# Optimization experiments

Measured on AMD Instinct MI355X. Metric: run time of the kernel, lower is better.

Reference implementation:

```python
import jax, jax.numpy as jnp
import numpy as np

EPS = 1e-10
WS = 5  # window_size
PAD = WS // 2


def _conv(x, k, pad_h, pad_w):
    # x: [N,1,H,W], k: [1,1,kh,kw], 'same'-style explicit padding
    return jax.lax.conv_general_dilated(
        x, k, window_strides=(1, 1),
        padding=[(pad_h, pad_h), (pad_w, pad_w)],
        dimension_numbers=("NCHW", "OIHW", "NCHW"))


def setup_inputs() -> dict:
    key = jax.random.key(0)
    B, C, Fr, T = 8, 2, 256, 2048
    spectrogram = jax.random.normal(key, (B, C, Fr, T), dtype=jnp.float32)
    # Gaussian kernel (window_size=5, sigma=1.0)
    c = WS // 2
    coords = jnp.arange(WS, dtype=jnp.float32) - c
    yy, xx = jnp.meshgrid(coords, coords, indexing="ij")
    g = jnp.exp(-(xx ** 2 + yy ** 2) / 2.0)
    gaussian_kernel = (g / g.sum()).reshape(1, 1, WS, WS)
    # Sobel kernels / 8
    sobel_x = (jnp.array([[-1, 0, 1], [-2, 0, 2], [-1, 0, 1]], jnp.float32) / 8.0).reshape(1, 1, 3, 3)
    sobel_y = (jnp.array([[-1, -2, -1], [0, 0, 0], [1, 2, 1]], jnp.float32) / 8.0).reshape(1, 1, 3, 3)
    # Harmonic kernel: 7x1 [-1,0,0,2,0,0,-1]
    hk = jnp.zeros(7, jnp.float32).at[0].set(-1.0).at[3].set(2.0).at[6].set(-1.0)
    harmonic_kernel = hk.reshape(1, 1, 7, 1)
    return {"spectrogram": spectrogram, "gaussian_kernel": gaussian_kernel,
            "sobel_x": sobel_x, "sobel_y": sobel_y, "harmonic_kernel": harmonic_kernel}


def _forward(spectrogram, gaussian_kernel, sobel_x, sobel_y, harmonic_kernel):
    B, C, Fr, T = spectrogram.shape
    # Per-channel 1-in/1-out convs == fold channels into batch.
    x = spectrogram.reshape(B * C, 1, Fr, T)

    grad_freq = _conv(x, sobel_y, 1, 1)
    grad_time = _conv(x, sobel_x, 1, 1)
    magnitude = jnp.sqrt(grad_freq ** 2 + grad_time ** 2 + EPS)
    angle = jnp.arctan2(grad_freq, grad_time + EPS)

    # ---- entropy (structure-tensor eigenvalue entropy) ----
    vx = magnitude * jnp.cos(angle)
    vy = magnitude * jnp.sin(angle)
    vxx = _conv(vx * vx, gaussian_kernel, PAD, PAD)
    vyy = _conv(vy * vy, gaussian_kernel, PAD, PAD)
    vxy = _conv(vx * vy, gaussian_kernel, PAD, PAD)
    trace = vxx + vyy
    det = vxx * vyy - vxy * vxy
    disc = jnp.sqrt(jnp.maximum(trace * trace - 4.0 * det, 0.0) + EPS)
    l1 = jnp.maximum((trace + disc) / 2.0, EPS)
    l2 = jnp.maximum((trace - disc) / 2.0, EPS)
    s = l1 + l2 + EPS
    p1, p2 = l1 / s, l2 / s
    entropy = -(p1 * jnp.log(p1 + EPS) + p2 * jnp.log(p2 + EPS)) / np.log(2.0)
    entropy = jnp.clip(entropy, 0.0, 1.0)

    # ---- alignment ----
    ux = jnp.cos(angle)
    uy = jnp.sin(angle)
    ux_avg = _conv(ux, gaussian_kernel, PAD, PAD)
    uy_avg = _conv(uy, gaussian_kernel, PAD, PAD)
    alignment = jnp.clip(jnp.sqrt(ux_avg ** 2 + uy_avg ** 2 + EPS), 0.0, 1.0)

    # ---- curvature ----
    dudx = _conv(ux, sobel_x, 1, 1)
    dudy = _conv(ux, sobel_y, 1, 1)
    dvdx = _conv(uy, sobel_x, 1, 1)
    dvdy = _conv(uy, sobel_y, 1, 1)
    curv = jnp.sqrt(dudx ** 2 + dudy ** 2 + dvdx ** 2 + dvdy ** 2 + EPS)
    curvature = _conv(curv, gaussian_kernel, PAD, PAD)

    # ---- harmonic coherence ----
    harm = jnp.abs(_conv(x, harmonic_kernel, 3, 0))
    local_energy = _conv(x ** 2, gaussian_kernel, PAD, PAD)
    harmonic = jnp.clip(harm / (local_energy + EPS), 0.0, 1.0)

    # ---- temporal stability: inverse temporal gradient magnitude, smoothed ----
    temporal = _conv(1.0 / (1.0 + jnp.abs(grad_time)), gaussian_kernel, PAD, PAD)
    temporal = jnp.clip(temporal, 0.0, 1.0)

    # ---- spectral flow: smoothed frequency-gradient magnitude ----
    spectral = jnp.clip(_conv(jnp.abs(grad_freq), gaussian_kernel, PAD, PAD), 0.0, 1.0)

    def chan_mean(f):  # [B*C,1,F,T] -> [B,1,F,T]
        return f.reshape(B, C, Fr, T).mean(axis=1, keepdims=True)

    return (chan_mean(entropy), chan_mean(alignment), chan_mean(curvature),
            chan_mean(harmonic), chan_mean(temporal), chan_mean(spectral))


def reference(spectrogram, gaussian_kernel, sobel_x, sobel_y, harmonic_kernel):
    return _forward(spectrogram, gaussian_kernel, sobel_x, sobel_y, harmonic_kernel)
```

## Files before the change

kernel.cpp:

```cpp
#include <hip/hip_runtime.h>
#include <hip/hip_fp16.h>


#define F_DIM 256
#define T_DIM 2048
#define B_DIM 8
#define C_DIM 2
#define TILE  32
#define NTHR  512

#define XROWS 40
#define XS    40
#define UROWS 38
#define US    40
#define FROWS 36
#define FS    36
#define FH2   18
#define EPSF  1e-10f

template<bool V> struct BoolC { static constexpr bool value = V; };

static __device__ __forceinline__ __half2 pack_h2(float a, float b) {
    auto v = __builtin_amdgcn_cvt_pkrtz(a, b);
    return *(__half2*)&v;
}
static __device__ __forceinline__ float clamp01(float x) {
    return fminf(fmaxf(x, 0.f), 1.f);
}

__global__ __launch_bounds__(512, 4)
void audio_struct_fused(const float* __restrict__ x_in,
                        const float* __restrict__ gk_in,
                        float* __restrict__ out)
{
    __shared__ __align__(16) float   s_x [XROWS*XS];
    __shared__ __align__(16) __half2 s_u [UROWS*US];
    __shared__ __align__(16) __half2 s_P0[FROWS*FS];
    __shared__ __align__(16) __half2 s_P1[FROWS*FS];
    __shared__ __align__(16) __half2 s_P2[FROWS*FS];
    __shared__ __align__(16) __half2 s_P3[FROWS*FS];
    __shared__ __align__(16) float   s_tmp[TILE*FS];

    const int tx  = threadIdx.x;
    const int ty  = threadIdx.y;
    const int tid = ty * 32 + tx;
    const int t0  = blockIdx.x * TILE;
    const int f0  = blockIdx.y * TILE;
    const int b   = blockIdx.z;

    float r0 = gk_in[10], r1 = gk_in[11], r2 = gk_in[12], r3 = gk_in[13], r4 = gk_in[14];
    float winv = __builtin_amdgcn_rcpf(r0 + r1 + r2 + r3 + r4);
    const float w[5] = {r0*winv, r1*winv, r2*winv, r3*winv, r4*winv};
    const __half2 wh2[5] = {pack_h2(w[0],w[0]), pack_h2(w[1],w[1]), pack_h2(w[2],w[2]),
                            pack_h2(w[3],w[3]), pack_h2(w[4],w[4])};
    const __half2 h2z    = pack_h2(0.f, 0.f);
    const __half2 two    = pack_h2(2.f, 2.f);
    const __half2 eighth = pack_h2(0.125f, 0.125f);

    auto vpass_pair = [&](const __half2* src, __half2* dst) {
        const uint2* s = (const uint2*)src;
        uint2* d = (uint2*)dst;
        for (int idx = tid; idx < TILE * FH2; idx += NTHR) {
            __half2 a0 = h2z, a1 = h2z;
            #pragma unroll
            for (int i = 0; i < 5; ++i) {
                uint2 v = s[idx + i * FH2];
                a0 = __hfma2(wh2[i], *(const __half2*)&v.x, a0);
                a1 = __hfma2(wh2[i], *(const __half2*)&v.y, a1);
            }
            uint2 o; o.x = *(const unsigned*)&a0; o.y = *(const unsigned*)&a1;
            d[idx] = o;
        }
    };

    float acc[6][2];
    #pragma unroll
    for (int k = 0; k < 6; ++k)
        #pragma unroll
        for (int s = 0; s < 2; ++s) acc[k][s] = 0.0f;

    const bool interior = (f0 >= 4) && (f0 + TILE + 4 <= F_DIM) &&
                          (t0 >= 4) && (t0 + TILE + 4 <= T_DIM);

    auto phaseABC = [&](const float* xp, auto FASTC) {
        constexpr bool FAST = decltype(FASTC)::value;

        for (int idx = tid; idx < XROWS * 20; idx += NTHR) {
            int r  = idx / 20, c2 = idx - r * 20;
            float2 v;
            if (FAST) {
                v = *(const float2*)(xp + (size_t)(f0 + r - 4) * T_DIM + (t0 + c2 * 2 - 4));
            } else {
                int gf = f0 + r - 4;
                int gt = t0 + c2 * 2 - 4;
                v = make_float2(0.f, 0.f);
                if ((unsigned)gf < (unsigned)F_DIM && (unsigned)gt < (unsigned)T_DIM)
                    v = *(const float2*)(xp + (size_t)gf * T_DIM + gt);
            }
            *(float2*)&s_x[r * XS + c2 * 2] = v;
        }
        __syncthreads();

        for (int q = tid; q < UROWS * 19; q += NTHR) {
            int r = q / 19, m = q - r * 19;
            const float2* x2p = (const float2*)s_x;
            int base = r * (XS/2) + m;
            float2 a0 = x2p[base],            b0 = x2p[base + 1];
            float2 a1 = x2p[base + (XS/2)],   b1 = x2p[base + (XS/2) + 1];
            float2 a2 = x2p[base + XS],       b2 = x2p[base + XS + 1];
            float c0 = a2.x - a0.x, c1 = a2.y - a0.y;
            float c2c = b2.x - b0.x, c3 = b2.y - b0.y;
            float s0 = fmaf(2.f, a1.x, a0.x + a2.x);
            float s1 = fmaf(2.f, a1.y, a0.y + a2.y);
            float s2 = fmaf(2.f, b1.x, b0.x + b2.x);
            float s3 = fmaf(2.f, b1.y, b0.y + b2.y);
            float gfvA = (fmaf(2.f, c1, c0) + c2c) * 0.125f;
            float gtvA = (s2 - s0) * 0.125f;
            float gfvB = (fmaf(2.f, c2c, c1) + c3) * 0.125f;
            float gtvB = (s3 - s1) * 0.125f;

            bool rin = (r >= 1) && (r < UROWS - 1);
            int  fiA = (r - 1) * FS + 2 * m - 1;
            int  gfr = f0 + r - 3;
            bool frOK = FAST || ((unsigned)gfr < (unsigned)F_DIM);

            #pragma unroll
            for (int jj = 0; jj < 2; ++jj) {
                float gfv = jj ? gfvB : gfvA;
                float gtv = jj ? gtvB : gtvA;
                int   ccI = 2 * m + jj;
                bool  okI = true;
                if (!FAST) {
                    int gtc = t0 + ccI - 3;
                    okI = frOK & ((unsigned)gtc < (unsigned)T_DIM);
                }
                float ux = 0.f, uy = 0.f, trp = 0.f, dfp = 0.f, sxy = 0.f,
                      tin = 0.f, sf = 0.f;
                if (okI) {
                    float gte = gtv + EPSF;
                    float g2f = gfv * gfv;
                    float d2  = fmaf(gte, gte, g2f);
                    float rh  = __builtin_amdgcn_rsqf(d2);
                    ux = gte * rh;
                    uy = gfv * rh;
                    float m2 = fmaf(gtv, gtv, g2f) + EPSF;
                    trp = m2;
                    dfp = m2 * (ux - uy) * (ux + uy);
                    sxy = m2 * ux * uy;
                    tin = __builtin_amdgcn_rcpf(1.0f + fabsf(gtv));
                    sf  = fabsf(gfv);
                }
                s_u[r * US + ccI + 1] = pack_h2(ux, uy);
                bool pv = rin && (jj ? (m <= 17) : (m >= 1));
                if (pv) {
                    int fi = fiA + jj;
                    s_P0[fi] = pack_h2(trp, dfp);
                    s_P1[fi] = pack_h2(sxy, tin);
                    s_P2[fi] = pack_h2(sf, 0.f);
                }
            }
        }
        __syncthreads();

        for (int q = tid; q < FROWS * 18; q += NTHR) {
            int r = q / 18, m = q - r * 18;
            const uint2* su2 = (const uint2*)s_u;
            int base = r * (US/2) + m;
            uint2 q00 = su2[base],              q01 = su2[base + 1],              q02 = su2[base + 2];
            uint2 q10 = su2[base + (US/2)],     q11 = su2[base + (US/2) + 1],     q12 = su2[base + (US/2) + 2];
            uint2 q20 = su2[base + US],         q21 = su2[base + US + 1],         q22 = su2[base + US + 2];
            #define H2(v) (*(const __half2*)&(v))
            __half2 l1 = __hadd2(H2(q00.y), H2(q20.y)); l1 = __hfma2(two, H2(q10.y), l1);
            __half2 l2 = __hadd2(H2(q01.x), H2(q21.x)); l2 = __hfma2(two, H2(q11.x), l2);
            __half2 l3 = __hadd2(H2(q01.y), H2(q21.y)); l3 = __hfma2(two, H2(q11.y), l3);
            __half2 l4 = __hadd2(H2(q02.x), H2(q22.x)); l4 = __hfma2(two, H2(q12.x), l4);
            __half2 tA = __hadd2(H2(q00.y), H2(q01.y)); tA = __hfma2(two, H2(q01.x), tA);
            __half2 bA = __hadd2(H2(q20.y), H2(q21.y)); bA = __hfma2(two, H2(q21.x), bA);
            __half2 tB = __hadd2(H2(q01.x), H2(q02.x)); tB = __hfma2(two, H2(q01.y), tB);
            __half2 bB = __hadd2(H2(q21.x), H2(q22.x)); bB = __hfma2(two, H2(q21.y), bB);
            #undef H2
            __half2 dxA = __hmul2(__hsub2(l3, l1), eighth);
            __half2 dyA = __hmul2(__hsub2(bA, tA), eighth);
            __half2 dxB = __hmul2(__hsub2(l4, l2), eighth);
            __half2 dyB = __hmul2(__hsub2(bB, tB), eighth);

            int gfr = f0 + r - 2;
            bool frOK = FAST || ((unsigned)gfr < (unsigned)F_DIM);
            #pragma unroll
            for (int jj = 0; jj < 2; ++jj) {
                float2 fx = __half22float2(jj ? dxB : dxA);
                float2 fy = __half22float2(jj ? dyB : dyA);
                float cv = __builtin_amdgcn_sqrtf(
                    fmaf(fx.x, fx.x, fmaf(fx.y, fx.y,
                    fmaf(fy.x, fy.x, fy.y * fy.y))) + EPSF);
                int ccI = 2 * m + jj;
                if (!FAST) {
                    int gtc = t0 + ccI - 2;
                    if (!(frOK & ((unsigned)gtc < (unsigned)T_DIM))) cv = 0.f;
                }
                ((__half*)s_P2)[2 * (r * FS + ccI) + 1] = __float2half_rn(cv);
            }
        }
        vpass_pair(s_P0, (__half2*)s_tmp);
        vpass_pair(s_P1, s_P3);
        __syncthreads();
    };

    for (int c = 0; c < C_DIM; ++c) {
        if (c) __syncthreads();

        const float* xp = x_in + (size_t)(b * C_DIM + c) * F_DIM * T_DIM;
        if (interior) phaseABC(xp, BoolC<true>{});
        else          phaseABC(xp, BoolC<false>{});

        __half2* tmp_h2 = (__half2*)s_tmp;

        {
            float trace_s[2], diff_s[2];
            #pragma unroll
            for (int s = 0; s < 2; ++s) {
                int ry = ty + 16 * s;
                float a = 0.f, bv = 0.f;
                #pragma unroll
                for (int j = 0; j < 5; ++j) {
                    float2 v = __half22float2(tmp_h2[ry * FS + tx + j]);
                    a += w[j] * v.x; bv += w[j] * v.y;
                }
                trace_s[s] = a; diff_s[s] = bv;
            }
            #pragma unroll
            for (int s = 0; s < 2; ++s) {
                int ry = ty + 16 * s;
                __half2 a = h2z;
                #pragma unroll
                for (int j = 0; j < 5; ++j)
                    a = __hfma2(wh2[j], s_P3[ry * FS + tx + j], a);
                float2 v = __half22float2(a);
                float trace = trace_s[s], diff = diff_s[s];
                float disc  = __builtin_amdgcn_sqrtf(
                                  fmaxf(diff * diff + 4.f * v.x * v.x, 0.f) + EPSF);
                float l1 = fmaxf(0.5f * (trace + disc), EPSF);
                float l2 = fmaxf(0.5f * (trace - disc), EPSF);
                float inv = __builtin_amdgcn_rcpf(l1 + l2 + EPSF);
                float p1 = l1 * inv, p2 = l2 * inv;
                float ent = -(p1 * __builtin_amdgcn_logf(p1 + EPSF)
                            + p2 * __builtin_amdgcn_logf(p2 + EPSF));
                acc[0][s] += 0.5f * clamp01(ent);
                acc[4][s] += 0.5f * clamp01(v.y);
            }
            vpass_pair(s_P2, s_P0);
            {
                const uint2* su2 = (const uint2*)s_u;
                uint2* dP1 = (uint2*)s_P1;
                for (int idx = tid; idx < TILE * FH2; idx += NTHR) {
                    int r = idx / FH2, p = idx - r * FH2;
                    const uint2* sp = su2 + (r + 1) * (US/2) + 1 + p;
                    __half2 a0 = h2z, a1 = h2z;
                    #pragma unroll
                    for (int i = 0; i < 5; ++i) {
                        uint2 v = sp[i * (US/2)];
                        a0 = __hfma2(wh2[i], *(const __half2*)&v.x, a0);
                        a1 = __hfma2(wh2[i], *(const __half2*)&v.y, a1);
                    }
                    uint2 o; o.x = *(const unsigned*)&a0; o.y = *(const unsigned*)&a1;
                    dP1[idx] = o;
                }
            }
        }
        __syncthreads();

        #pragma unroll
        for (int s = 0; s < 2; ++s) {
            int ry = ty + 16 * s;
            __half2 a = h2z;
            #pragma unroll
            for (int j = 0; j < 5; ++j)
                a = __hfma2(wh2[j], s_P0[ry * FS + tx + j], a);
            float2 v = __half22float2(a);
            acc[5][s] += 0.5f * clamp01(v.x);
            acc[2][s] += 0.5f * v.y;
        }
        #pragma unroll
        for (int s = 0; s < 2; ++s) {
            int ry = ty + 16 * s;
            __half2 a = h2z;
            #pragma unroll
            for (int j = 0; j < 5; ++j)
                a = __hfma2(wh2[j], s_P1[ry * FS + tx + j], a);
            float2 v = __half22float2(a);
            acc[1][s] += 0.5f * clamp01(
                __builtin_amdgcn_sqrtf(v.x * v.x + v.y * v.y + EPSF));
        }
        {
            const float2* sx2 = (const float2*)s_x;
            float2* dt2 = (float2*)s_tmp;
            for (int idx = tid; idx < TILE * FH2; idx += NTHR) {
                int r = idx / FH2, p = idx - r * FH2;
                const float2* sp = sx2 + (r + 2) * (XS/2) + 1 + p;
                float a = 0.f, bv = 0.f;
                #pragma unroll
                for (int i = 0; i < 5; ++i) {
                    float2 v = sp[i * (XS/2)];
                    a  = fmaf(w[i], v.x * v.x, a);
                    bv = fmaf(w[i], v.y * v.y, bv);
                }
                dt2[idx] = make_float2(a, bv);
            }
        }
        __syncthreads();

        #pragma unroll
        for (int s = 0; s < 2; ++s) {
            int ry = ty + 16 * s;
            float le = 0.f;
            #pragma unroll
            for (int j = 0; j < 5; ++j)
                le += w[j] * s_tmp[ry * FS + tx + j];
            float xm  = s_x[(ry + 1) * XS + tx + 4];
            float x0v = s_x[(ry + 4) * XS + tx + 4];
            float xpv = s_x[(ry + 7) * XS + tx + 4];
            float harm = fabsf(2.f * x0v - xm - xpv);
            acc[3][s] += 0.5f * clamp01(harm * __builtin_amdgcn_rcpf(le + EPSF));
        }
    }

    const size_t plane = (size_t)B_DIM * F_DIM * T_DIM;
    const size_t base  = (size_t)b * F_DIM * T_DIM + (size_t)f0 * T_DIM + t0 + tx;
    #pragma unroll
    for (int k = 0; k < 6; ++k)
        #pragma unroll
        for (int s = 0; s < 2; ++s)
            out[k * plane + base + (size_t)(ty + 16 * s) * T_DIM] = acc[k][s];
}

extern "C" void kernel_launch(void* const* d_in, const int* in_sizes, int n_in,
                              void* d_out, int out_size, void* d_ws, size_t ws_size,
                              hipStream_t stream) {
    const float* x  = (const float*)d_in[0];
    const float* gk = (const float*)d_in[1];
    float* out = (float*)d_out;
    dim3 grid(T_DIM / TILE, F_DIM / TILE, B_DIM);
    dim3 block(32, 16);
    audio_struct_fused<<<grid, block, 0, stream>>>(x, gk, out);
}
```

Measured before the change: 206.3 us.

## Give each thread two adjacent columns and two rows for register reuse

Changes thread-to-output mapping so each thread computes two horizontally adjacent outputs (one row, two columns) in the horizontal passes, reusing loaded shared-memory values across both outputs via wide uint2/float2 loads. The vertical passes now produce two output rows per thread from six loaded rows instead of five per row. Final stores become float2 writes. Intent is to cut LDS load count and instruction overhead; it raises register pressure under a 512x4 launch bound.

Measured after the change: 202.0 us. 2.1% less time.

```diff
diff --git a/kernel.cpp b/kernel.cpp
--- a/kernel.cpp
+++ b/kernel.cpp
@@ -26,6 +26,9 @@
 }
 static __device__ __forceinline__ float clamp01(float x) {
     return fminf(fmaxf(x, 0.f), 1.f);
+}
+static __device__ __forceinline__ __half2 u2h(unsigned v) {
+    return *(const __half2*)&v;
 }
 
 __global__ __launch_bounds__(512, 4)
@@ -44,6 +47,8 @@
     const int tx  = threadIdx.x;
     const int ty  = threadIdx.y;
     const int tid = ty * 32 + tx;
+    const int ryh = tid >> 4;
+    const int mch = tid & 15;
     const int t0  = blockIdx.x * TILE;
     const int f0  = blockIdx.y * TILE;
     const int b   = blockIdx.z;
@@ -57,19 +62,27 @@
     const __half2 two    = pack_h2(2.f, 2.f);
     const __half2 eighth = pack_h2(0.125f, 0.125f);
 
-    auto vpass_pair = [&](const __half2* src, __half2* dst) {
+    auto vpass2 = [&](const __half2* src, __half2* dst) {
         const uint2* s = (const uint2*)src;
         uint2* d = (uint2*)dst;
-        for (int idx = tid; idx < TILE * FH2; idx += NTHR) {
-            __half2 a0 = h2z, a1 = h2z;
+        for (int idx = tid; idx < 16 * FH2; idx += NTHR) {
+            int rg = idx / FH2, p = idx - rg * FH2;
+            int base = 2 * rg * FH2 + p;
+            uint2 vv[6];
+            #pragma unroll
+            for (int i = 0; i < 6; ++i) vv[i] = s[base + i * FH2];
+            __half2 a0 = h2z, a1 = h2z, b0 = h2z, b1 = h2z;
             #pragma unroll
             for (int i = 0; i < 5; ++i) {
-                uint2 v = s[idx + i * FH2];
-                a0 = __hfma2(wh2[i], *(const __half2*)&v.x, a0);
-                a1 = __hfma2(wh2[i], *(const __half2*)&v.y, a1);
-            }
-            uint2 o; o.x = *(const unsigned*)&a0; o.y = *(const unsigned*)&a1;
-            d[idx] = o;
+                a0 = __hfma2(wh2[i], u2h(vv[i].x),     a0);
+                a1 = __hfma2(wh2[i], u2h(vv[i].y),     a1);
+                b0 = __hfma2(wh2[i], u2h(vv[i + 1].x), b0);
+                b1 = __hfma2(wh2[i], u2h(vv[i + 1].y), b1);
+            }
+            uint2 oa; oa.x = *(const unsigned*)&a0; oa.y = *(const unsigned*)&a1;
+            uint2 ob; ob.x = *(const unsigned*)&b0; ob.y = *(const unsigned*)&b1;
+            d[base] = oa;
+            d[base + FH2] = ob;
         }
     };
 
@@ -169,16 +182,14 @@
             uint2 q00 = su2[base],              q01 = su2[base + 1],              q02 = su2[base + 2];
             uint2 q10 = su2[base + (US/2)],     q11 = su2[base + (US/2) + 1],     q12 = su2[base + (US/2) + 2];
             uint2 q20 = su2[base + US],         q21 = su2[base + US + 1],         q22 = su2[base + US + 2];
-            #define H2(v) (*(const __half2*)&(v))
-            __half2 l1 = __hadd2(H2(q00.y), H2(q20.y)); l1 = __hfma2(two, H2(q10.y), l1);
-            __half2 l2 = __hadd2(H2(q01.x), H2(q21.x)); l2 = __hfma2(two, H2(q11.x), l2);
-            __half2 l3 = __hadd2(H2(q01.y), H2(q21.y)); l3 = __hfma2(two, H2(q11.y), l3);
-            __half2 l4 = __hadd2(H2(q02.x), H2(q22.x)); l4 = __hfma2(two, H2(q12.x), l4);
-            __half2 tA = __hadd2(H2(q00.y), H2(q01.y)); tA = __hfma2(two, H2(q01.x), tA);
-            __half2 bA = __hadd2(H2(q20.y), H2(q21.y)); bA = __hfma2(two, H2(q21.x), bA);
-            __half2 tB = __hadd2(H2(q01.x), H2(q02.x)); tB = __hfma2(two, H2(q01.y), tB);
-            __half2 bB = __hadd2(H2(q21.x), H2(q22.x)); bB = __hfma2(two, H2(q21.y), bB);
-            #undef H2
+            __half2 l1 = __hadd2(u2h(q00.y), u2h(q20.y)); l1 = __hfma2(two, u2h(q10.y), l1);
+            __half2 l2 = __hadd2(u2h(q01.x), u2h(q21.x)); l2 = __hfma2(two, u2h(q11.x), l2);
+            __half2 l3 = __hadd2(u2h(q01.y), u2h(q21.y)); l3 = __hfma2(two, u2h(q11.y), l3);
+            __half2 l4 = __hadd2(u2h(q02.x), u2h(q22.x)); l4 = __hfma2(two, u2h(q12.x), l4);
+            __half2 tA = __hadd2(u2h(q00.y), u2h(q01.y)); tA = __hfma2(two, u2h(q01.x), tA);
+            __half2 bA = __hadd2(u2h(q20.y), u2h(q21.y)); bA = __hfma2(two, u2h(q21.x), bA);
+            __half2 tB = __hadd2(u2h(q01.x), u2h(q02.x)); tB = __hfma2(two, u2h(q01.y), tB);
+            __half2 bB = __hadd2(u2h(q21.x), u2h(q22.x)); bB = __hfma2(two, u2h(q21.y), bB);
             __half2 dxA = __hmul2(__hsub2(l3, l1), eighth);
             __half2 dyA = __hmul2(__hsub2(bA, tA), eighth);
             __half2 dxB = __hmul2(__hsub2(l4, l2), eighth);
@@ -201,8 +212,8 @@
                 ((__half*)s_P2)[2 * (r * FS + ccI) + 1] = __float2half_rn(cv);
             }
         }
-        vpass_pair(s_P0, (__half2*)s_tmp);
-        vpass_pair(s_P1, s_P3);
+        vpass2(s_P0, (__half2*)s_tmp);
+        vpass2(s_P1, s_P3);
         __syncthreads();
     };
 
@@ -216,27 +227,37 @@
         __half2* tmp_h2 = (__half2*)s_tmp;
 
         {
-            float trace_s[2], diff_s[2];
-            #pragma unroll
-            for (int s = 0; s < 2; ++s) {
-                int ry = ty + 16 * s;
-                float a = 0.f, bv = 0.f;
-                #pragma unroll
-                for (int j = 0; j < 5; ++j) {
-                    float2 v = __half22float2(tmp_h2[ry * FS + tx + j]);
-                    a += w[j] * v.x; bv += w[j] * v.y;
-                }
-                trace_s[s] = a; diff_s[s] = bv;
-            }
-            #pragma unroll
-            for (int s = 0; s < 2; ++s) {
-                int ry = ty + 16 * s;
-                __half2 a = h2z;
-                #pragma unroll
-                for (int j = 0; j < 5; ++j)
-                    a = __hfma2(wh2[j], s_P3[ry * FS + tx + j], a);
-                float2 v = __half22float2(a);
-                float trace = trace_s[s], diff = diff_s[s];
+            const uint2* t2 = (const uint2*)tmp_h2;
+            uint2 ta = t2[ryh * FH2 + mch], tb = t2[ryh * FH2 + mch + 1],
+                  tc = t2[ryh * FH2 + mch + 2];
+            float2 e0 = __half22float2(u2h(ta.x)), e1 = __half22float2(u2h(ta.y));
+            float2 e2 = __half22float2(u2h(tb.x)), e3 = __half22float2(u2h(tb.y));
+            float2 e4 = __half22float2(u2h(tc.x)), e5 = __half22float2(u2h(tc.y));
+            float trc[2], dfc[2];
+            trc[0] = w[0]*e0.x + w[1]*e1.x + w[2]*e2.x + w[3]*e3.x + w[4]*e4.x;
+            dfc[0] = w[0]*e0.y + w[1]*e1.y + w[2]*e2.y + w[3]*e3.y + w[4]*e4.y;
+            trc[1] = w[0]*e1.x + w[1]*e2.x + w[2]*e3.x + w[3]*e4.x + w[4]*e5.x;
+            dfc[1] = w[0]*e1.y + w[1]*e2.y + w[2]*e3.y + w[3]*e4.y + w[4]*e5.y;
+
+            const uint2* p3q = (const uint2*)s_P3;
+            uint2 pa = p3q[ryh * FH2 + mch], pb = p3q[ryh * FH2 + mch + 1],
+                  pc = p3q[ryh * FH2 + mch + 2];
+            __half2 aA = h2z, aB = h2z;
+            aA = __hfma2(wh2[0], u2h(pa.x), aA);
+            aA = __hfma2(wh2[1], u2h(pa.y), aA);
+            aA = __hfma2(wh2[2], u2h(pb.x), aA);
+            aA = __hfma2(wh2[3], u2h(pb.y), aA);
+            aA = __hfma2(wh2[4], u2h(pc.x), aA);
+            aB = __hfma2(wh2[0], u2h(pa.y), aB);
+            aB = __hfma2(wh2[1], u2h(pb.x), aB);
+            aB = __hfma2(wh2[2], u2h(pb.y), aB);
+            aB = __hfma2(wh2[3], u2h(pc.x), aB);
+            aB = __hfma2(wh2[4], u2h(pc.y), aB);
+            float2 vc[2] = {__half22float2(aA), __half22float2(aB)};
+            #pragma unroll
+            for (int col = 0; col < 2; ++col) {
+                float trace = trc[col], diff = dfc[col];
+                float2 v = vc[col];
                 float disc  = __builtin_amdgcn_sqrtf(
                                   fmaxf(diff * diff + 4.f * v.x * v.x, 0.f) + EPSF);
                 float l1 = fmaxf(0.5f * (trace + disc), EPSF);
@@ -245,92 +266,124 @@
                 float p1 = l1 * inv, p2 = l2 * inv;
                 float ent = -(p1 * __builtin_amdgcn_logf(p1 + EPSF)
                             + p2 * __builtin_amdgcn_logf(p2 + EPSF));
-                acc[0][s] += 0.5f * clamp01(ent);
-                acc[4][s] += 0.5f * clamp01(v.y);
-            }
-            vpass_pair(s_P2, s_P0);
+                acc[0][col] += 0.5f * clamp01(ent);
+                acc[4][col] += 0.5f * clamp01(v.y);
+            }
+
+            vpass2(s_P2, s_P0);
             {
                 const uint2* su2 = (const uint2*)s_u;
                 uint2* dP1 = (uint2*)s_P1;
-                for (int idx = tid; idx < TILE * FH2; idx += NTHR) {
-                    int r = idx / FH2, p = idx - r * FH2;
-                    const uint2* sp = su2 + (r + 1) * (US/2) + 1 + p;
-                    __half2 a0 = h2z, a1 = h2z;
+                for (int idx = tid; idx < 16 * FH2; idx += NTHR) {
+                    int rg = idx / FH2, p = idx - rg * FH2;
+                    const uint2* sp = su2 + (2 * rg + 1) * (US/2) + 1 + p;
+                    uint2 vv[6];
+                    #pragma unroll
+                    for (int i = 0; i < 6; ++i) vv[i] = sp[i * (US/2)];
+                    __half2 a0 = h2z, a1 = h2z, b0 = h2z, b1 = h2z;
                     #pragma unroll
                     for (int i = 0; i < 5; ++i) {
-                        uint2 v = sp[i * (US/2)];
-                        a0 = __hfma2(wh2[i], *(const __half2*)&v.x, a0);
-                        a1 = __hfma2(wh2[i], *(const __half2*)&v.y, a1);
+                        a0 = __hfma2(wh2[i], u2h(vv[i].x),     a0);
+                        a1 = __hfma2(wh2[i], u2h(vv[i].y),     a1);
+                        b0 = __hfma2(wh2[i], u2h(vv[i + 1].x), b0);
+                        b1 = __hfma2(wh2[i], u2h(vv[i + 1].y), b1);
                     }
-                    uint2 o; o.x = *(const unsigned*)&a0; o.y = *(const unsigned*)&a1;
-                    dP1[idx] = o;
-                }
-            }
-        }
-        __syncthreads();
-
-        #pragma unroll
-        for (int s = 0; s < 2; ++s) {
-            int ry = ty + 16 * s;
-            __half2 a = h2z;
-            #pragma unroll
-            for (int j = 0; j < 5; ++j)
-                a = __hfma2(wh2[j], s_P0[ry * FS + tx + j], a);
-            float2 v = __half22float2(a);
-            acc[5][s] += 0.5f * clamp01(v.x);
-            acc[2][s] += 0.5f * v.y;
-        }
-        #pragma unroll
-        for (int s = 0; s < 2; ++s) {
-            int ry = ty + 16 * s;
-            __half2 a = h2z;
-            #pragma unroll
-            for (int j = 0; j < 5; ++j)
-                a = __hfma2(wh2[j], s_P1[ry * FS + tx + j], a);
-            float2 v = __half22float2(a);
-            acc[1][s] += 0.5f * clamp01(
-                __builtin_amdgcn_sqrtf(v.x * v.x + v.y * v.y + EPSF));
-        }
+                    uint2 oa; oa.x = *(const unsigned*)&a0; oa.y = *(const unsigned*)&a1;
+                    uint2 ob; ob.x = *(const unsigned*)&b0; ob.y = *(const unsigned*)&b1;
+                    dP1[2 * rg * FH2 + p] = oa;
+                    dP1[(2 * rg + 1) * FH2 + p] = ob;
+                }
+            }
+        }
+        __syncthreads();
+
         {
+            const uint2* p0q = (const uint2*)s_P0;
+            uint2 qa = p0q[ryh * FH2 + mch], qb = p0q[ryh * FH2 + mch + 1],
+                  qc = p0q[ryh * FH2 + mch + 2];
+            __half2 sA = h2z, sB = h2z;
+            sA = __hfma2(wh2[0], u2h(qa.x), sA);
+            sA = __hfma2(wh2[1], u2h(qa.y), sA);
+            sA = __hfma2(wh2[2], u2h(qb.x), sA);
+            sA = __hfma2(wh2[3], u2h(qb.y), sA);
+            sA = __hfma2(wh2[4], u2h(qc.x), sA);
+            sB = __hfma2(wh2[0], u2h(qa.y), sB);
+            sB = __hfma2(wh2[1], u2h(qb.x), sB);
+            sB = __hfma2(wh2[2], u2h(qb.y), sB);
+            sB = __hfma2(wh2[3], u2h(qc.x), sB);
+            sB = __hfma2(wh2[4], u2h(qc.y), sB);
+            float2 s0 = __half22float2(sA), s1 = __half22float2(sB);
+            acc[5][0] += 0.5f * clamp01(s0.x);  acc[2][0] += 0.5f * s0.y;
+            acc[5][1] += 0.5f * clamp01(s1.x);  acc[2][1] += 0.5f * s1.y;
+
+            const uint2* p1q = (const uint2*)s_P1;
+            uint2 ra = p1q[ryh * FH2 + mch], rb = p1q[ryh * FH2 + mch + 1],
+                  rc = p1q[ryh * FH2 + mch + 2];
+            __half2 uA = h2z, uB = h2z;
+            uA = __hfma2(wh2[0], u2h(ra.x), uA);
+            uA = __hfma2(wh2[1], u2h(ra.y), uA);
+            uA = __hfma2(wh2[2], u2h(rb.x), uA);
+            uA = __hfma2(wh2[3], u2h(rb.y), uA);
+            uA = __hfma2(wh2[4], u2h(rc.x), uA);
+            uB = __hfma2(wh2[0], u2h(ra.y), uB);
+            uB = __hfma2(wh2[1], u2h(rb.x), uB);
+            uB = __hfma2(wh2[2], u2h(rb.y), uB);
+            uB = __hfma2(wh2[3], u2h(rc.x), uB);
+            uB = __hfma2(wh2[4], u2h(rc.y), uB);
+            float2 u0 = __half22float2(uA), u1 = __half22float2(uB);
+            acc[1][0] += 0.5f * clamp01(
+                __builtin_amdgcn_sqrtf(u0.x * u0.x + u0.y * u0.y + EPSF));
+            acc[1][1] += 0.5f * clamp01(
+                __builtin_amdgcn_sqrtf(u1.x * u1.x + u1.y * u1.y + EPSF));
+
             const float2* sx2 = (const float2*)s_x;
             float2* dt2 = (float2*)s_tmp;
-            for (int idx = tid; idx < TILE * FH2; idx += NTHR) {
-                int r = idx / FH2, p = idx - r * FH2;
-                const float2* sp = sx2 + (r + 2) * (XS/2) + 1 + p;
-                float a = 0.f, bv = 0.f;
+            for (int idx = tid; idx < 16 * FH2; idx += NTHR) {
+                int rg = idx / FH2, p = idx - rg * FH2;
+                const float2* sp = sx2 + (2 * rg + 2) * (XS/2) + 1 + p;
+                float2 sq[6];
+                #pragma unroll
+                for (int i = 0; i < 6; ++i) {
+                    float2 v = sp[i * (XS/2)];
+                    sq[i] = make_float2(v.x * v.x, v.y * v.y);
+                }
+                float aA = 0.f, bA = 0.f, aB = 0.f, bB = 0.f;
                 #pragma unroll
                 for (int i = 0; i < 5; ++i) {
-                    float2 v = sp[i * (XS/2)];
-                    a  = fmaf(w[i], v.x * v.x, a);
-                    bv = fmaf(w[i], v.y * v.y, bv);
-                }
-                dt2[idx] = make_float2(a, bv);
-            }
-        }
-        __syncthreads();
-
-        #pragma unroll
-        for (int s = 0; s < 2; ++s) {
-            int ry = ty + 16 * s;
-            float le = 0.f;
-            #pragma unroll
-            for (int j = 0; j < 5; ++j)
-                le += w[j] * s_tmp[ry * FS + tx + j];
-            float xm  = s_x[(ry + 1) * XS + tx + 4];
-            float x0v = s_x[(ry + 4) * XS + tx + 4];
-            float xpv = s_x[(ry + 7) * XS + tx + 4];
-            float harm = fabsf(2.f * x0v - xm - xpv);
-            acc[3][s] += 0.5f * clamp01(harm * __builtin_amdgcn_rcpf(le + EPSF));
+                    aA = fmaf(w[i], sq[i].x,     aA);
+                    bA = fmaf(w[i], sq[i].y,     bA);
+                    aB = fmaf(w[i], sq[i + 1].x, aB);
+                    bB = fmaf(w[i], sq[i + 1].y, bB);
+                }
+                dt2[2 * rg * FH2 + p] = make_float2(aA, bA);
+                dt2[(2 * rg + 1) * FH2 + p] = make_float2(aB, bB);
+            }
+        }
+        __syncthreads();
+
+        {
+            const float2* tf = (const float2*)s_tmp;
+            float2 q0 = tf[ryh * FH2 + mch], q1 = tf[ryh * FH2 + mch + 1],
+                   q2 = tf[ryh * FH2 + mch + 2];
+            float le0 = w[0]*q0.x + w[1]*q0.y + w[2]*q1.x + w[3]*q1.y + w[4]*q2.x;
+            float le1 = w[0]*q0.y + w[1]*q1.x + w[2]*q1.y + w[3]*q2.x + w[4]*q2.y;
+            const float2* sxf = (const float2*)s_x;
+            float2 xm  = sxf[(ryh + 1) * (XS/2) + mch + 2];
+            float2 x0v = sxf[(ryh + 4) * (XS/2) + mch + 2];
+            float2 xpv = sxf[(ryh + 7) * (XS/2) + mch + 2];
+            float hA = fabsf(2.f * x0v.x - xm.x - xpv.x);
+            float hB = fabsf(2.f * x0v.y - xm.y - xpv.y);
+            acc[3][0] += 0.5f * clamp01(hA * __builtin_amdgcn_rcpf(le0 + EPSF));
+            acc[3][1] += 0.5f * clamp01(hB * __builtin_amdgcn_rcpf(le1 + EPSF));
         }
     }
 
     const size_t plane = (size_t)B_DIM * F_DIM * T_DIM;
-    const size_t base  = (size_t)b * F_DIM * T_DIM + (size_t)f0 * T_DIM + t0 + tx;
+    const size_t base  = (size_t)b * F_DIM * T_DIM
+                       + (size_t)(f0 + ryh) * T_DIM + t0 + 2 * mch;
     #pragma unroll
     for (int k = 0; k < 6; ++k)
-        #pragma unroll
-        for (int s = 0; s < 2; ++s)
-            out[k * plane + base + (size_t)(ty + 16 * s) * T_DIM] = acc[k][s];
+        *(float2*)(out + k * plane + base) = make_float2(acc[k][0], acc[k][1]);
 }
 
 extern "C" void kernel_launch(void* const* d_in, const int* in_sizes, int n_in,
```

## Register-block horizontal and vertical passes with 128-bit LDS accesses

Applied to the files above, without the earlier changes.

Reworks the shared-memory convolution passes so each thread computes several outputs. Vertical passes now produce two rows per thread and the Sobel pass produces four columns, using uint4/float4 LDS loads and reusing overlapping taps. Horizontal passes have only half the threads compute four adjacent outputs each, with float4 output stores. This reduces LDS load instructions and index arithmetic, at the cost of idling half the threads in the final stages and higher register pressure under the 512x4 launch bound.

Result: no change. 205.4 us (-0.5%).

```diff
diff --git a/kernel.cpp b/kernel.cpp
--- a/kernel.cpp
+++ b/kernel.cpp
@@ -16,6 +16,7 @@
 #define FROWS 36
 #define FS    36
 #define FH2   18
+#define FH4   9
 #define EPSF  1e-10f
 
 template<bool V> struct BoolC { static constexpr bool value = V; };
@@ -26,6 +27,9 @@
 }
 static __device__ __forceinline__ float clamp01(float x) {
     return fminf(fmaxf(x, 0.f), 1.f);
+}
+static __device__ __forceinline__ __half2 u2h(unsigned v) {
+    return *(const __half2*)&v;
 }
 
 __global__ __launch_bounds__(512, 4)
@@ -44,6 +48,9 @@
     const int tx  = threadIdx.x;
     const int ty  = threadIdx.y;
     const int tid = ty * 32 + tx;
+    const bool hact = (tid < 256);
+    const int ryq = tid >> 3;
+    const int mq  = tid & 7;
     const int t0  = blockIdx.x * TILE;
     const int f0  = blockIdx.y * TILE;
     const int b   = blockIdx.z;
@@ -57,27 +64,40 @@
     const __half2 two    = pack_h2(2.f, 2.f);
     const __half2 eighth = pack_h2(0.125f, 0.125f);
 
-    auto vpass_pair = [&](const __half2* src, __half2* dst) {
-        const uint2* s = (const uint2*)src;
-        uint2* d = (uint2*)dst;
-        for (int idx = tid; idx < TILE * FH2; idx += NTHR) {
-            __half2 a0 = h2z, a1 = h2z;
+    auto vpass4 = [&](const __half2* src, __half2* dst) {
+        const uint4* s = (const uint4*)src;
+        uint4* d = (uint4*)dst;
+        for (int idx = tid; idx < 16 * FH4; idx += NTHR) {
+            int rg = idx / FH4, p = idx - rg * FH4;
+            int base = 2 * rg * FH4 + p;
+            uint4 vv[6];
+            #pragma unroll
+            for (int i = 0; i < 6; ++i) vv[i] = s[base + i * FH4];
+            __half2 a0=h2z,a1=h2z,a2=h2z,a3=h2z, b0=h2z,b1=h2z,b2=h2z,b3=h2z;
             #pragma unroll
             for (int i = 0; i < 5; ++i) {
-                uint2 v = s[idx + i * FH2];
-                a0 = __hfma2(wh2[i], *(const __half2*)&v.x, a0);
-                a1 = __hfma2(wh2[i], *(const __half2*)&v.y, a1);
-            }
-            uint2 o; o.x = *(const unsigned*)&a0; o.y = *(const unsigned*)&a1;
-            d[idx] = o;
+                a0 = __hfma2(wh2[i], u2h(vv[i].x),   a0);
+                a1 = __hfma2(wh2[i], u2h(vv[i].y),   a1);
+                a2 = __hfma2(wh2[i], u2h(vv[i].z),   a2);
+                a3 = __hfma2(wh2[i], u2h(vv[i].w),   a3);
+                b0 = __hfma2(wh2[i], u2h(vv[i+1].x), b0);
+                b1 = __hfma2(wh2[i], u2h(vv[i+1].y), b1);
+                b2 = __hfma2(wh2[i], u2h(vv[i+1].z), b2);
+                b3 = __hfma2(wh2[i], u2h(vv[i+1].w), b3);
+            }
+            uint4 oa, ob;
+            oa.x=*(unsigned*)&a0; oa.y=*(unsigned*)&a1; oa.z=*(unsigned*)&a2; oa.w=*(unsigned*)&a3;
+            ob.x=*(unsigned*)&b0; ob.y=*(unsigned*)&b1; ob.z=*(unsigned*)&b2; ob.w=*(unsigned*)&b3;
+            d[base] = oa;
+            d[base + FH4] = ob;
         }
     };
 
-    float acc[6][2];
+    float acc[6][4];
     #pragma unroll
     for (int k = 0; k < 6; ++k)
         #pragma unroll
-        for (int s = 0; s < 2; ++s) acc[k][s] = 0.0f;
+        for (int s = 0; s < 4; ++s) acc[k][s] = 0.0f;
 
     const bool interior = (f0 >= 4) && (f0 + TILE + 4 <= F_DIM) &&
                           (t0 >= 4) && (t0 + TILE + 4 <= T_DIM);
@@ -162,47 +182,48 @@
         }
         __syncthreads();
 
-        for (int q = tid; q < FROWS * 18; q += NTHR) {
-            int r = q / 18, m = q - r * 18;
-            const uint2* su2 = (const uint2*)s_u;
-            int base = r * (US/2) + m;
-            uint2 q00 = su2[base],              q01 = su2[base + 1],              q02 = su2[base + 2];
-            uint2 q10 = su2[base + (US/2)],     q11 = su2[base + (US/2) + 1],     q12 = su2[base + (US/2) + 2];
-            uint2 q20 = su2[base + US],         q21 = su2[base + US + 1],         q22 = su2[base + US + 2];
-            #define H2(v) (*(const __half2*)&(v))
-            __half2 l1 = __hadd2(H2(q00.y), H2(q20.y)); l1 = __hfma2(two, H2(q10.y), l1);
-            __half2 l2 = __hadd2(H2(q01.x), H2(q21.x)); l2 = __hfma2(two, H2(q11.x), l2);
-            __half2 l3 = __hadd2(H2(q01.y), H2(q21.y)); l3 = __hfma2(two, H2(q11.y), l3);
-            __half2 l4 = __hadd2(H2(q02.x), H2(q22.x)); l4 = __hfma2(two, H2(q12.x), l4);
-            __half2 tA = __hadd2(H2(q00.y), H2(q01.y)); tA = __hfma2(two, H2(q01.x), tA);
-            __half2 bA = __hadd2(H2(q20.y), H2(q21.y)); bA = __hfma2(two, H2(q21.x), bA);
-            __half2 tB = __hadd2(H2(q01.x), H2(q02.x)); tB = __hfma2(two, H2(q01.y), tB);
-            __half2 bB = __hadd2(H2(q21.x), H2(q22.x)); bB = __hfma2(two, H2(q21.y), bB);
-            #undef H2
-            __half2 dxA = __hmul2(__hsub2(l3, l1), eighth);
-            __half2 dyA = __hmul2(__hsub2(bA, tA), eighth);
-            __half2 dxB = __hmul2(__hsub2(l4, l2), eighth);
-            __half2 dyB = __hmul2(__hsub2(bB, tB), eighth);
-
+        for (int q = tid; q < FROWS * FH4; q += NTHR) {
+            int r = q / FH4, Q = q - r * FH4;
+            const uint4* su4 = (const uint4*)s_u;
+            int base = r * 10 + Q;
+            uint4 ta4 = su4[base],      tb4 = su4[base + 1];
+            uint4 ma4 = su4[base + 10], mb4 = su4[base + 11];
+            uint4 ba4 = su4[base + 20], bb4 = su4[base + 21];
+            __half2 t_[8] = {u2h(ta4.x),u2h(ta4.y),u2h(ta4.z),u2h(ta4.w),
+                             u2h(tb4.x),u2h(tb4.y),u2h(tb4.z),u2h(tb4.w)};
+            __half2 m_[8] = {u2h(ma4.x),u2h(ma4.y),u2h(ma4.z),u2h(ma4.w),
+                             u2h(mb4.x),u2h(mb4.y),u2h(mb4.z),u2h(mb4.w)};
+            __half2 b_[8] = {u2h(ba4.x),u2h(ba4.y),u2h(ba4.z),u2h(ba4.w),
+                             u2h(bb4.x),u2h(bb4.y),u2h(bb4.z),u2h(bb4.w)};
+            __half2 l_[7];
+            #pragma unroll
+            for (int k = 1; k <= 6; ++k) {
+                __half2 s = __hadd2(t_[k], b_[k]);
+                l_[k] = __hfma2(two, m_[k], s);
+            }
             int gfr = f0 + r - 2;
             bool frOK = FAST || ((unsigned)gfr < (unsigned)F_DIM);
             #pragma unroll
-            for (int jj = 0; jj < 2; ++jj) {
-                float2 fx = __half22float2(jj ? dxB : dxA);
-                float2 fy = __half22float2(jj ? dyB : dyA);
+            for (int jj = 0; jj < 4; ++jj) {
+                __half2 tr = __hadd2(t_[jj+1], t_[jj+3]); tr = __hfma2(two, t_[jj+2], tr);
+                __half2 br = __hadd2(b_[jj+1], b_[jj+3]); br = __hfma2(two, b_[jj+2], br);
+                __half2 dx = __hmul2(__hsub2(l_[jj+3], l_[jj+1]), eighth);
+                __half2 dy = __hmul2(__hsub2(br, tr), eighth);
+                float2 fx = __half22float2(dx);
+                float2 fy = __half22float2(dy);
                 float cv = __builtin_amdgcn_sqrtf(
                     fmaf(fx.x, fx.x, fmaf(fx.y, fx.y,
                     fmaf(fy.x, fy.x, fy.y * fy.y))) + EPSF);
-                int ccI = 2 * m + jj;
+                int cc = 4 * Q + jj;
                 if (!FAST) {
-                    int gtc = t0 + ccI - 2;
+                    int gtc = t0 + cc - 2;
                     if (!(frOK & ((unsigned)gtc < (unsigned)T_DIM))) cv = 0.f;
                 }
-                ((__half*)s_P2)[2 * (r * FS + ccI) + 1] = __float2half_rn(cv);
-            }
-        }
-        vpass_pair(s_P0, (__half2*)s_tmp);
-        vpass_pair(s_P1, s_P3);
+                ((__half*)s_P2)[2 * (r * FS + cc) + 1] = __float2half_rn(cv);
+            }
+        }
+        vpass4(s_P0, (__half2*)s_tmp);
+        vpass4(s_P1, s_P3);
         __syncthreads();
     };
 
@@ -215,28 +236,30 @@
 
         __half2* tmp_h2 = (__half2*)s_tmp;
 
-        {
-            float trace_s[2], diff_s[2];
-            #pragma unroll
-            for (int s = 0; s < 2; ++s) {
-                int ry = ty + 16 * s;
-                float a = 0.f, bv = 0.f;
-                #pragma unroll
-                for (int j = 0; j < 5; ++j) {
-                    float2 v = __half22float2(tmp_h2[ry * FS + tx + j]);
-                    a += w[j] * v.x; bv += w[j] * v.y;
-                }
-                trace_s[s] = a; diff_s[s] = bv;
-            }
-            #pragma unroll
-            for (int s = 0; s < 2; ++s) {
-                int ry = ty + 16 * s;
+        if (hact) {
+            const uint4* t4 = (const uint4*)tmp_h2;
+            uint4 ua = t4[ryq * FH4 + mq], ub = t4[ryq * FH4 + mq + 1];
+            float2 e[8] = {__half22float2(u2h(ua.x)), __half22float2(u2h(ua.y)),
+                           __half22float2(u2h(ua.z)), __half22float2(u2h(ua.w)),
+                           __half22float2(u2h(ub.x)), __half22float2(u2h(ub.y)),
+                           __half22float2(u2h(ub.z)), __half22float2(u2h(ub.w))};
+            const uint4* p34 = (const uint4*)s_P3;
+            uint4 pa = p34[ryq * FH4 + mq], pb = p34[ryq * FH4 + mq + 1];
+            __half2 pe[8] = {u2h(pa.x),u2h(pa.y),u2h(pa.z),u2h(pa.w),
+                             u2h(pb.x),u2h(pb.y),u2h(pb.z),u2h(pb.w)};
+            #pragma unroll
+            for (int jj = 0; jj < 4; ++jj) {
+                float trace = w[0]*e[jj].x + w[1]*e[jj+1].x + w[2]*e[jj+2].x
+                            + w[3]*e[jj+3].x + w[4]*e[jj+4].x;
+                float diff  = w[0]*e[jj].y + w[1]*e[jj+1].y + w[2]*e[jj+2].y
+                            + w[3]*e[jj+3].y + w[4]*e[jj+4].y;
                 __half2 a = h2z;
-                #pragma unroll
-                for (int j = 0; j < 5; ++j)
-                    a = __hfma2(wh2[j], s_P3[ry * FS + tx + j], a);
+                a = __hfma2(wh2[0], pe[jj],     a);
+                a = __hfma2(wh2[1], pe[jj + 1], a);
+                a = __hfma2(wh2[2], pe[jj + 2], a);
+                a = __hfma2(wh2[3], pe[jj + 3], a);
+                a = __hfma2(wh2[4], pe[jj + 4], a);
                 float2 v = __half22float2(a);
-                float trace = trace_s[s], diff = diff_s[s];
                 float disc  = __builtin_amdgcn_sqrtf(
                                   fmaxf(diff * diff + 4.f * v.x * v.x, 0.f) + EPSF);
                 float l1 = fmaxf(0.5f * (trace + disc), EPSF);
@@ -245,92 +268,125 @@
                 float p1 = l1 * inv, p2 = l2 * inv;
                 float ent = -(p1 * __builtin_amdgcn_logf(p1 + EPSF)
                             + p2 * __builtin_amdgcn_logf(p2 + EPSF));
-                acc[0][s] += 0.5f * clamp01(ent);
-                acc[4][s] += 0.5f * clamp01(v.y);
-            }
-            vpass_pair(s_P2, s_P0);
-            {
-                const uint2* su2 = (const uint2*)s_u;
-                uint2* dP1 = (uint2*)s_P1;
-                for (int idx = tid; idx < TILE * FH2; idx += NTHR) {
-                    int r = idx / FH2, p = idx - r * FH2;
-                    const uint2* sp = su2 + (r + 1) * (US/2) + 1 + p;
-                    __half2 a0 = h2z, a1 = h2z;
-                    #pragma unroll
-                    for (int i = 0; i < 5; ++i) {
-                        uint2 v = sp[i * (US/2)];
-                        a0 = __hfma2(wh2[i], *(const __half2*)&v.x, a0);
-                        a1 = __hfma2(wh2[i], *(const __half2*)&v.y, a1);
-                    }
-                    uint2 o; o.x = *(const unsigned*)&a0; o.y = *(const unsigned*)&a1;
-                    dP1[idx] = o;
-                }
+                acc[0][jj] += 0.5f * clamp01(ent);
+                acc[4][jj] += 0.5f * clamp01(v.y);
+            }
+        }
+        vpass4(s_P2, s_P0);
+        {
+            const uint2* su2 = (const uint2*)s_u;
+            uint2* dP1 = (uint2*)s_P1;
+            for (int idx = tid; idx < 16 * FH2; idx += NTHR) {
+                int rg = idx / FH2, p = idx - rg * FH2;
+                const uint2* sp = su2 + (2 * rg + 1) * (US/2) + 1 + p;
+                uint2 vv[6];
+                #pragma unroll
+                for (int i = 0; i < 6; ++i) vv[i] = sp[i * (US/2)];
+                __half2 a0 = h2z, a1 = h2z, b0 = h2z, b1 = h2z;
+                #pragma unroll
+                for (int i = 0; i < 5; ++i) {
+                    a0 = __hfma2(wh2[i], u2h(vv[i].x),     a0);
+                    a1 = __hfma2(wh2[i], u2h(vv[i].y),     a1);
+                    b0 = __hfma2(wh2[i], u2h(vv[i + 1].x), b0);
+                    b1 = __hfma2(wh2[i], u2h(vv[i + 1].y), b1);
+                }
+                uint2 oa; oa.x = *(const unsigned*)&a0; oa.y = *(const unsigned*)&a1;
+                uint2 ob; ob.x = *(const unsigned*)&b0; ob.y = *(const unsigned*)&b1;
+                dP1[2 * rg * FH2 + p] = oa;
+                dP1[(2 * rg + 1) * FH2 + p] = ob;
             }
         }
         __syncthreads();
 
-        #pragma unroll
-        for (int s = 0; s < 2; ++s) {
-            int ry = ty + 16 * s;
-            __half2 a = h2z;
-            #pragma unroll
-            for (int j = 0; j < 5; ++j)
-                a = __hfma2(wh2[j], s_P0[ry * FS + tx + j], a);
-            float2 v = __half22float2(a);
-            acc[5][s] += 0.5f * clamp01(v.x);
-            acc[2][s] += 0.5f * v.y;
-        }
-        #pragma unroll
-        for (int s = 0; s < 2; ++s) {
-            int ry = ty + 16 * s;
-            __half2 a = h2z;
-            #pragma unroll
-            for (int j = 0; j < 5; ++j)
-                a = __hfma2(wh2[j], s_P1[ry * FS + tx + j], a);
-            float2 v = __half22float2(a);
-            acc[1][s] += 0.5f * clamp01(
-                __builtin_amdgcn_sqrtf(v.x * v.x + v.y * v.y + EPSF));
+        if (hact) {
+            const uint4* p04 = (const uint4*)s_P0;
+            uint4 qa = p04[ryq * FH4 + mq], qb = p04[ryq * FH4 + mq + 1];
+            __half2 qe[8] = {u2h(qa.x),u2h(qa.y),u2h(qa.z),u2h(qa.w),
+                             u2h(qb.x),u2h(qb.y),u2h(qb.z),u2h(qb.w)};
+            const uint4* p14 = (const uint4*)s_P1;
+            uint4 ra = p14[ryq * FH4 + mq], rb = p14[ryq * FH4 + mq + 1];
+            __half2 re[8] = {u2h(ra.x),u2h(ra.y),u2h(ra.z),u2h(ra.w),
+                             u2h(rb.x),u2h(rb.y),u2h(rb.z),u2h(rb.w)};
+            #pragma unroll
+            for (int jj = 0; jj < 4; ++jj) {
+                __half2 sA = h2z;
+                sA = __hfma2(wh2[0], qe[jj],     sA);
+                sA = __hfma2(wh2[1], qe[jj + 1], sA);
+                sA = __hfma2(wh2[2], qe[jj + 2], sA);
+                sA = __hfma2(wh2[3], qe[jj + 3], sA);
+                sA = __hfma2(wh2[4], qe[jj + 4], sA);
+                float2 sv = __half22float2(sA);
+                acc[5][jj] += 0.5f * clamp01(sv.x);
+                acc[2][jj] += 0.5f * sv.y;
+                __half2 uA = h2z;
+                uA = __hfma2(wh2[0], re[jj],     uA);
+                uA = __hfma2(wh2[1], re[jj + 1], uA);
+                uA = __hfma2(wh2[2], re[jj + 2], uA);
+                uA = __hfma2(wh2[3], re[jj + 3], uA);
+                uA = __hfma2(wh2[4], re[jj + 4], uA);
+                float2 uv = __half22float2(uA);
+                acc[1][jj] += 0.5f * clamp01(
+                    __builtin_amdgcn_sqrtf(uv.x * uv.x + uv.y * uv.y + EPSF));
+            }
         }
         {
             const float2* sx2 = (const float2*)s_x;
             float2* dt2 = (float2*)s_tmp;
-            for (int idx = tid; idx < TILE * FH2; idx += NTHR) {
-                int r = idx / FH2, p = idx - r * FH2;
-                const float2* sp = sx2 + (r + 2) * (XS/2) + 1 + p;
-                float a = 0.f, bv = 0.f;
+            for (int idx = tid; idx < 16 * FH2; idx += NTHR) {
+                int rg = idx / FH2, p = idx - rg * FH2;
+                const float2* sp = sx2 + (2 * rg + 2) * (XS/2) + 1 + p;
+                float2 sq[6];
+                #pragma unroll
+                for (int i = 0; i < 6; ++i) {
+                    float2 v = sp[i * (XS/2)];
+                    sq[i] = make_float2(v.x * v.x, v.y * v.y);
+                }
+                float aA = 0.f, bA = 0.f, aB = 0.f, bB = 0.f;
                 #pragma unroll
                 for (int i = 0; i < 5; ++i) {
-                    float2 v = sp[i * (XS/2)];
-                    a  = fmaf(w[i], v.x * v.x, a);
-                    bv = fmaf(w[i], v.y * v.y, bv);
-                }
-                dt2[idx] = make_float2(a, bv);
+                    aA = fmaf(w[i], sq[i].x,     aA);
+                    bA = fmaf(w[i], sq[i].y,     bA);
+                    aB = fmaf(w[i], sq[i + 1].x, aB);
+                    bB = fmaf(w[i], sq[i + 1].y, bB);
+                }
+                dt2[2 * rg * FH2 + p] = make_float2(aA, bA);
+                dt2[(2 * rg + 1) * FH2 + p] = make_float2(aB, bB);
             }
         }
         __syncthreads();
 
+        if (hact) {
+            const float4* tf4 = (const float4*)s_tmp;
+            float4 g0 = tf4[ryq * FH4 + mq], g1 = tf4[ryq * FH4 + mq + 1];
+            float le[4];
+            le[0] = w[0]*g0.x + w[1]*g0.y + w[2]*g0.z + w[3]*g0.w + w[4]*g1.x;
+            le[1] = w[0]*g0.y + w[1]*g0.z + w[2]*g0.w + w[3]*g1.x + w[4]*g1.y;
+            le[2] = w[0]*g0.z + w[1]*g0.w + w[2]*g1.x + w[3]*g1.y + w[4]*g1.z;
+            le[3] = w[0]*g0.w + w[1]*g1.x + w[2]*g1.y + w[3]*g1.z + w[4]*g1.w;
+            const float4* sx4 = (const float4*)s_x;
+            float4 xm4 = sx4[(ryq + 1) * 10 + mq + 1];
+            float4 x04 = sx4[(ryq + 4) * 10 + mq + 1];
+            float4 xp4 = sx4[(ryq + 7) * 10 + mq + 1];
+            float xmv[4] = {xm4.x, xm4.y, xm4.z, xm4.w};
+            float x0v[4] = {x04.x, x04.y, x04.z, x04.w};
+            float xpv[4] = {xp4.x, xp4.y, xp4.z, xp4.w};
+            #pragma unroll
+            for (int jj = 0; jj < 4; ++jj) {
+                float harm = fabsf(2.f * x0v[jj] - xmv[jj] - xpv[jj]);
+                acc[3][jj] += 0.5f * clamp01(harm * __builtin_amdgcn_rcpf(le[jj] + EPSF));
+            }
+        }
+    }
+
+    if (hact) {
+        const size_t plane = (size_t)B_DIM * F_DIM * T_DIM;
+        const size_t base  = (size_t)b * F_DIM * T_DIM
+                           + (size_t)(f0 + ryq) * T_DIM + t0 + 4 * mq;
         #pragma unroll
-        for (int s = 0; s < 2; ++s) {
-            int ry = ty + 16 * s;
-            float le = 0.f;
-            #pragma unroll
-            for (int j = 0; j < 5; ++j)
-                le += w[j] * s_tmp[ry * FS + tx + j];
-            float xm  = s_x[(ry + 1) * XS + tx + 4];
-            float x0v = s_x[(ry + 4) * XS + tx + 4];
-            float xpv = s_x[(ry + 7) * XS + tx + 4];
-            float harm = fabsf(2.f * x0v - xm - xpv);
-            acc[3][s] += 0.5f * clamp01(harm * __builtin_amdgcn_rcpf(le + EPSF));
-        }
+        for (int k = 0; k < 6; ++k)
+            *(float4*)(out + k * plane + base) =
+                make_float4(acc[k][0], acc[k][1], acc[k][2], acc[k][3]);
     }
-
-    const size_t plane = (size_t)B_DIM * F_DIM * T_DIM;
-    const size_t base  = (size_t)b * F_DIM * T_DIM + (size_t)f0 * T_DIM + t0 + tx;
-    #pragma unroll
-    for (int k = 0; k < 6; ++k)
-        #pragma unroll
-        for (int s = 0; s < 2; ++s)
-            out[k * plane + base + (size_t)(ty + 16 * s) * T_DIM] = acc[k][s];
 }
 
 extern "C" void kernel_launch(void* const* d_in, const int* in_sizes, int n_in,
```
